# Kernel optimization log

Hardware: AMD Instinct MI355X
Metric: run time of the kernel (lower is better)

## Reference

```python
import jax, jax.numpy as jnp
import numpy as np

NUM_SPARSE = 26
VOCAB = 100000
EMB = 64
B = 2048
DENSE = 13
NUM_FEA = NUM_SPARSE + 1  # 26 embeddings + bottom-MLP output


def _xavier(key, shape):
    fan_in, fan_out = shape[0], shape[1]
    lim = jnp.sqrt(6.0 / (fan_in + fan_out))
    return jax.random.uniform(key, shape, jnp.float32, -lim, lim)


def setup_inputs() -> dict:
    key = jax.random.key(0)
    ks = jax.random.split(key, 20)
    inp = {
        "dense": jax.random.normal(ks[0], (B, DENSE), jnp.float32),
        "cat_idx": jax.random.randint(ks[1], (B, NUM_SPARSE), 0, VOCAB, jnp.int32),
        # stacked EmbeddingBag tables (all same vocab -> one [26, V, 64] tensor)
        "tables": _xavier(ks[2], (VOCAB, EMB))[None] * jnp.ones((NUM_SPARSE, 1, 1), jnp.float32) * 0
                  + jax.random.normal(ks[3], (NUM_SPARSE, VOCAB, EMB), jnp.float32) * 0.01,
        # bottom MLP: 13 -> 512 -> 256 -> 64
        "bw0": _xavier(ks[4], (DENSE, 512)), "bb0": jnp.zeros((512,), jnp.float32),
        "bw1": _xavier(ks[5], (512, 256)),   "bb1": jnp.zeros((256,), jnp.float32),
        "bw2": _xavier(ks[6], (256, EMB)),   "bb2": jnp.zeros((EMB,), jnp.float32),
        # top MLP: 415 -> 1024 -> 512 -> 256 -> 1
        "tw0": _xavier(ks[7], (EMB + NUM_FEA * (NUM_FEA - 1) // 2, 1024)), "tb0": jnp.zeros((1024,), jnp.float32),
        "tw1": _xavier(ks[8], (1024, 512)),  "tb1": jnp.zeros((512,), jnp.float32),
        "tw2": _xavier(ks[9], (512, 256)),   "tb2": jnp.zeros((256,), jnp.float32),
        "tw3": _xavier(ks[10], (256, 1)),    "tb3": jnp.zeros((1,), jnp.float32),
    }
    return inp


def reference(dense, cat_idx, tables, bw0, bb0, bw1, bb1, bw2, bb2,
              tw0, tb0, tw1, tb1, tw2, tb2, tw3, tb3):
    # bottom MLP on dense features -> [B, EMB]
    h = jax.nn.relu(dense @ bw0 + bb0)
    h = jax.nn.relu(h @ bw1 + bb1)
    bot = jax.nn.relu(h @ bw2 + bb2)

    # EmbeddingBag (single index per bag, sum mode == plain gather): [B, 26, EMB]
    feat_ids = jnp.arange(NUM_SPARSE)[None, :]  # [1, 26]
    emb = tables[feat_ids, cat_idx]             # [B, 26, EMB]

    # dot interaction: batched Gram matrix then lower-triangular gather
    T = jnp.concatenate([bot[:, None, :], emb], axis=1)  # [B, 27, EMB]
    Z = jnp.einsum("bif,bjf->bij", T, T)                  # [B, 27, 27]
    li, lj = np.tril_indices(NUM_FEA, k=-1)               # 351 pairs
    Zflat = Z[:, li, lj]                                  # [B, 351]

    R = jnp.concatenate([bot, Zflat], axis=1)             # [B, 415]

    # top MLP
    r = jax.nn.relu(R @ tw0 + tb0)
    r = jax.nn.relu(r @ tw1 + tb1)
    r = jax.nn.relu(r @ tw2 + tb2)
    out = jax.nn.sigmoid(r @ tw3 + tb3)                   # [B, 1]
    return out
```

## Files before the change

### kernel.cpp

```cpp
#include <hip/hip_runtime.h>
#include <hip/hip_bf16.h>


#define BATCH 2048
#define VOCAB 100000
#define EMB 64
#define NSPARSE 26
#define NFEA 27
#define NPAIR 351
#define RLD 448

typedef __attribute__((ext_vector_type(8))) __bf16 bf16x8;
typedef __attribute__((ext_vector_type(4))) float f32x4;
typedef __hip_bfloat16 bf16;

#define GLOAD16(g, l)                                                          \
    __builtin_amdgcn_global_load_lds(                                          \
        (const __attribute__((address_space(1))) unsigned int*)(g),            \
        (__attribute__((address_space(3))) unsigned int*)(l), 16, 0, 0)

template<int BK, bool DENSEPAD>
__global__ __launch_bounds__(256) void gemm_bf16(
    const void* __restrict__ Araw,
    const bf16* __restrict__ Wt,
    const float* __restrict__ bias,
    bf16* __restrict__ C,
    int M, int N, int K, int ldC)
{
    constexpr int ROWB   = BK * 2;
    constexpr int SLOTS  = BK / 8;
    constexpr int PASSES = BK / 32;
    constexpr int RPP    = 256 / SLOTS;

    __shared__ __align__(16) bf16 As[64 * BK];
    __shared__ __align__(16) bf16 Bs[64 * BK];

    const int t   = threadIdx.x;
    const int nbn = N >> 6;
    const int bm  = blockIdx.x / nbn;
    const int bn  = blockIdx.x % nbn;
    const int row0 = bm << 6, n0 = bn << 6;

    const int wid  = t >> 6, lane = t & 63;
    const int wr   = wid >> 1, wc = wid & 1;
    const int lr   = lane & 15;
    const int q    = lane >> 4;

#define SWZ(row, s) ((BK == 64) ? ((s) ^ ((row) & 7)) : ((s) ^ (((row) >> 1) & 3)))

    const int srow  = t / SLOTS;
    const int sslot = t % SLOTS;

    const bf16* Ab[PASSES];
    const bf16* Bb[PASSES];
#pragma unroll
    for (int p = 0; p < PASSES; ++p) {
        const int r = p * RPP + srow;
        const int g = SWZ(r, sslot);
        if (!DENSEPAD)
            Ab[p] = (const bf16*)Araw + (size_t)(row0 + r) * K + g * 8;
        Bb[p] = Wt + (size_t)(n0 + r) * K + g * 8;
    }

    f32x4 acc[2][2] = {};

    for (int k0 = 0; k0 < K; k0 += BK) {
        if (DENSEPAD) {
            const float* Df = (const float*)Araw;
#pragma unroll
            for (int idx = t; idx < 64 * 32; idx += 256) {
                const int r = idx >> 5, c = idx & 31;
                const float v = (c < 13) ? Df[(size_t)(row0 + r) * 13 + c] : 0.f;
                As[r * 32 + SWZ(r, c >> 3) * 8 + (c & 7)] = __float2bfloat16(v);
            }
        } else {
#pragma unroll
            for (int p = 0; p < PASSES; ++p)
                GLOAD16(Ab[p] + k0, (char*)As + p * 4096 + t * 16);
        }
#pragma unroll
        for (int p = 0; p < PASSES; ++p)
            GLOAD16(Bb[p] + k0, (char*)Bs + p * 4096 + t * 16);
        __syncthreads();

        bf16x8 af[PASSES][2], bfr[PASSES][2];
#pragma unroll
        for (int kk = 0; kk < PASSES; ++kk) {
#pragma unroll
            for (int m = 0; m < 2; ++m) {
                const int r = wr * 32 + 16 * m + lr;
                af[kk][m] = *(const bf16x8*)((const char*)As + r * ROWB +
                                             SWZ(r, kk * 4 + q) * 16);
            }
#pragma unroll
            for (int n = 0; n < 2; ++n) {
                const int r = wc * 32 + 16 * n + lr;
                bfr[kk][n] = *(const bf16x8*)((const char*)Bs + r * ROWB +
                                              SWZ(r, kk * 4 + q) * 16);
            }
        }
#pragma unroll
        for (int kk = 0; kk < PASSES; ++kk)
#pragma unroll
            for (int m = 0; m < 2; ++m)
#pragma unroll
                for (int n = 0; n < 2; ++n)
                    acc[m][n] = __builtin_amdgcn_mfma_f32_16x16x32_bf16(
                        af[kk][m], bfr[kk][n], acc[m][n], 0, 0, 0);
        __syncthreads();
    }
#undef SWZ

#pragma unroll
    for (int n = 0; n < 2; ++n) {
        const int col = n0 + wc * 32 + 16 * n + lr;
        const float bv = bias[col];
#pragma unroll
        for (int m = 0; m < 2; ++m) {
#pragma unroll
            for (int i = 0; i < 4; ++i) {
                const int row = row0 + wr * 32 + 16 * m + q * 4 + i;
                float v = acc[m][n][i] + bv;
                v = fmaxf(v, 0.f);
                C[(size_t)row * ldC + col] = __float2bfloat16(v);
            }
        }
    }
}

struct WConvArgs {
    const float* src[6];
    bf16*        dst[6];
    int K[6], N[6], Kp[6], t0[7];
};

__global__ __launch_bounds__(256) void wconv_kernel(WConvArgs a)
{
    __shared__ float Ts[32][33];
    int w = 0;
    while (w < 5 && (int)blockIdx.x >= a.t0[w + 1]) ++w;
    const int rel = blockIdx.x - a.t0[w];
    const int K = a.K[w], N = a.N[w], Kp = a.Kp[w];
    const int nbn = N >> 5;
    const int tk = rel / nbn, tn = rel % nbn;
    const int tx = threadIdx.x & 31, ty = threadIdx.x >> 5;

    const float* src = a.src[w];
    bf16* dst = a.dst[w];

#pragma unroll
    for (int rr = 0; rr < 4; ++rr) {
        const int k = tk * 32 + ty + rr * 8;
        const int n = tn * 32 + tx;
        Ts[ty + rr * 8][tx] = (k < K) ? src[(size_t)k * N + n] : 0.f;
    }
    __syncthreads();
#pragma unroll
    for (int rr = 0; rr < 4; ++rr) {
        const int n = tn * 32 + ty + rr * 8;
        const int kp = tk * 32 + tx;
        dst[(size_t)n * Kp + kp] = __float2bfloat16(Ts[tx][ty + rr * 8]);
    }
}

__global__ __launch_bounds__(256) void interact_kernel(
    const int* __restrict__ cat_idx, const float* __restrict__ tables,
    bf16* __restrict__ R)
{
    __shared__ float T[NFEA][EMB + 1];

    const int b    = blockIdx.x;
    const int t    = threadIdx.x;
    const int g    = t >> 6;
    const int lane = t & 63;
    bf16* Rrow = R + (size_t)b * RLD;

    for (int f = g; f < NFEA; f += 4) {
        if (f == 0) {
            T[0][lane] = __bfloat162float(Rrow[lane]);
        } else {
            const int j   = f - 1;
            const int idx = cat_idx[b * NSPARSE + j];
            T[f][lane] = tables[((size_t)j * VOCAB + idx) * EMB + lane];
        }
    }
    __syncthreads();

    if (t < RLD - 415) Rrow[415 + t] = __float2bfloat16(0.f);

    for (int p = t; p < NPAIR; p += 256) {
        int i = (int)((1.0f + sqrtf(1.0f + 8.0f * (float)p)) * 0.5f);
        while (i * (i - 1) / 2 > p) --i;
        while ((i + 1) * i / 2 <= p) ++i;
        const int j = p - i * (i - 1) / 2;
        float s = 0.f;
#pragma unroll 16
        for (int k = 0; k < EMB; ++k) s += T[i][k] * T[j][k];
        Rrow[EMB + p] = __float2bfloat16(s);
    }
}

__global__ __launch_bounds__(256) void top3_kernel(
    const bf16* __restrict__ A, const float* __restrict__ w,
    const float* __restrict__ bias, float* __restrict__ out)
{
    const int gid  = blockIdx.x * 256 + threadIdx.x;
    const int row  = gid >> 6;
    const int lane = gid & 63;

    const bf16* arow = A + (size_t)row * 256;
    float s = 0.f;
#pragma unroll
    for (int k = lane; k < 256; k += 64)
        s += __bfloat162float(arow[k]) * w[k];
#pragma unroll
    for (int off = 32; off; off >>= 1) s += __shfl_down(s, off);
    if (lane == 0) out[row] = 1.f / (1.f + expf(-(s + bias[0])));
}

extern "C" void kernel_launch(void* const* d_in, const int* in_sizes, int n_in,
                              void* d_out, int out_size, void* d_ws, size_t ws_size,
                              hipStream_t stream)
{
    const float* dense   = (const float*)d_in[0];
    const int*   cat_idx = (const int*)  d_in[1];
    const float* tables  = (const float*)d_in[2];
    const float* bw0 = (const float*)d_in[3];
    const float* bb0 = (const float*)d_in[4];
    const float* bw1 = (const float*)d_in[5];
    const float* bb1 = (const float*)d_in[6];
    const float* bw2 = (const float*)d_in[7];
    const float* bb2 = (const float*)d_in[8];
    const float* tw0 = (const float*)d_in[9];
    const float* tb0 = (const float*)d_in[10];
    const float* tw1 = (const float*)d_in[11];
    const float* tb1 = (const float*)d_in[12];
    const float* tw2 = (const float*)d_in[13];
    const float* tb2 = (const float*)d_in[14];
    const float* tw3 = (const float*)d_in[15];
    const float* tb3 = (const float*)d_in[16];

    bf16* p = (bf16*)d_ws;
    bf16* h0   = p; p += (size_t)BATCH * 512;
    bf16* h1   = p; p += (size_t)BATCH * 256;
    bf16* R    = p; p += (size_t)BATCH * RLD;
    bf16* r0   = p; p += (size_t)BATCH * 1024;
    bf16* r1   = p; p += (size_t)BATCH * 512;
    bf16* r2   = p; p += (size_t)BATCH * 256;
    bf16* bw0t = p; p += 512 * 32;
    bf16* bw1t = p; p += 256 * 512;
    bf16* bw2t = p; p += 64 * 256;
    bf16* tw0t = p; p += 1024 * RLD;
    bf16* tw1t = p; p += 512 * 1024;
    bf16* tw2t = p; p += 256 * 512;
    float* out = (float*)d_out;

    WConvArgs wa;
    wa.src[0] = bw0;  wa.dst[0] = bw0t; wa.K[0] = 13;   wa.N[0] = 512;  wa.Kp[0] = 32;
    wa.src[1] = bw1;  wa.dst[1] = bw1t; wa.K[1] = 512;  wa.N[1] = 256;  wa.Kp[1] = 512;
    wa.src[2] = bw2;  wa.dst[2] = bw2t; wa.K[2] = 256;  wa.N[2] = 64;   wa.Kp[2] = 256;
    wa.src[3] = tw0;  wa.dst[3] = tw0t; wa.K[3] = 415;  wa.N[3] = 1024; wa.Kp[3] = RLD;
    wa.src[4] = tw1;  wa.dst[4] = tw1t; wa.K[4] = 1024; wa.N[4] = 512;  wa.Kp[4] = 1024;
    wa.src[5] = tw2;  wa.dst[5] = tw2t; wa.K[5] = 512;  wa.N[5] = 256;  wa.Kp[5] = 512;
    int tiles = 0;
    for (int w = 0; w < 6; ++w) {
        wa.t0[w] = tiles;
        tiles += (wa.Kp[w] >> 5) * (wa.N[w] >> 5);
    }
    wa.t0[6] = tiles;

    wconv_kernel<<<tiles, 256, 0, stream>>>(wa);

    gemm_bf16<32, true ><<<(BATCH / 64) * (512 / 64), 256, 0, stream>>>(
        dense, bw0t, bb0, h0, BATCH, 512, 32, 512);
    gemm_bf16<64, false><<<(BATCH / 64) * (256 / 64), 256, 0, stream>>>(
        h0, bw1t, bb1, h1, BATCH, 256, 512, 256);
    gemm_bf16<64, false><<<(BATCH / 64) * (64 / 64), 256, 0, stream>>>(
        h1, bw2t, bb2, R, BATCH, 64, 256, RLD);

    interact_kernel<<<BATCH, 256, 0, stream>>>(cat_idx, tables, R);

    gemm_bf16<64, false><<<(BATCH / 64) * (1024 / 64), 256, 0, stream>>>(
        R, tw0t, tb0, r0, BATCH, 1024, RLD, 1024);
    gemm_bf16<64, false><<<(BATCH / 64) * (512 / 64), 256, 0, stream>>>(
        r0, tw1t, tb1, r1, BATCH, 512, 1024, 512);
    gemm_bf16<64, false><<<(BATCH / 64) * (256 / 64), 256, 0, stream>>>(
        r1, tw2t, tb2, r2, BATCH, 256, 512, 256);
    top3_kernel<<<BATCH / 4, 256, 0, stream>>>(r2, tw3, tb3, out);
}
```

Baseline: 67.74 us.

## Double-buffer GEMM LDS tiles and fuse bottom-MLP last layer into interaction

The GEMM kernel now double-buffers its A/B shared-memory tiles, prefetching the next K slice while computing on the current one, with one barrier per iteration. The final bottom-MLP layer (256->64) is removed as a separate GEMM launch and computed inside the interaction kernel with scalar FMAs from bf16 h1 and transposed weights. The interaction kernel also processes 8 batch rows per block with vectorized float4 embedding gathers. This saves a kernel launch and a round trip of the bottom output, but adds scalar dot-product work and far more shared memory per block (about 56KB for T), which may reduce occupancy.

```diff
diff --git a/kernel.cpp b/kernel.cpp
--- a/kernel.cpp
+++ b/kernel.cpp
@@ -19,6 +19,11 @@
         (const __attribute__((address_space(1))) unsigned int*)(g),            \
         (__attribute__((address_space(3))) unsigned int*)(l), 16, 0, 0)
 
+template<int BK>
+__device__ __forceinline__ int swz(int row, int s) {
+    return (BK == 64) ? (s ^ (row & 7)) : (s ^ ((row >> 1) & 3));
+}
+
 template<int BK, bool DENSEPAD>
 __global__ __launch_bounds__(256) void gemm_bf16(
     const void* __restrict__ Araw,
@@ -32,8 +37,8 @@
     constexpr int PASSES = BK / 32;
     constexpr int RPP    = 256 / SLOTS;
 
-    __shared__ __align__(16) bf16 As[64 * BK];
-    __shared__ __align__(16) bf16 Bs[64 * BK];
+    __shared__ __align__(16) bf16 As[2][64 * BK];
+    __shared__ __align__(16) bf16 Bs[2][64 * BK];
 
     const int t   = threadIdx.x;
     const int nbn = N >> 6;
@@ -46,8 +51,6 @@
     const int lr   = lane & 15;
     const int q    = lane >> 4;
 
-#define SWZ(row, s) ((BK == 64) ? ((s) ^ ((row) & 7)) : ((s) ^ (((row) >> 1) & 3)))
-
     const int srow  = t / SLOTS;
     const int sslot = t % SLOTS;
 
@@ -56,32 +59,40 @@
 #pragma unroll
     for (int p = 0; p < PASSES; ++p) {
         const int r = p * RPP + srow;
-        const int g = SWZ(r, sslot);
+        const int g = swz<BK>(r, sslot);
         if (!DENSEPAD)
             Ab[p] = (const bf16*)Araw + (size_t)(row0 + r) * K + g * 8;
         Bb[p] = Wt + (size_t)(n0 + r) * K + g * 8;
     }
 
-    f32x4 acc[2][2] = {};
-
-    for (int k0 = 0; k0 < K; k0 += BK) {
-        if (DENSEPAD) {
+    auto stage = [&](int k0, int buf) {
+        if constexpr (DENSEPAD) {
             const float* Df = (const float*)Araw;
 #pragma unroll
             for (int idx = t; idx < 64 * 32; idx += 256) {
                 const int r = idx >> 5, c = idx & 31;
                 const float v = (c < 13) ? Df[(size_t)(row0 + r) * 13 + c] : 0.f;
-                As[r * 32 + SWZ(r, c >> 3) * 8 + (c & 7)] = __float2bfloat16(v);
+                As[buf][r * 32 + swz<BK>(r, c >> 3) * 8 + (c & 7)] =
+                    __float2bfloat16(v);
             }
         } else {
 #pragma unroll
             for (int p = 0; p < PASSES; ++p)
-                GLOAD16(Ab[p] + k0, (char*)As + p * 4096 + t * 16);
+                GLOAD16(Ab[p] + k0, (char*)As[buf] + p * 4096 + t * 16);
         }
 #pragma unroll
         for (int p = 0; p < PASSES; ++p)
-            GLOAD16(Bb[p] + k0, (char*)Bs + p * 4096 + t * 16);
-        __syncthreads();
+            GLOAD16(Bb[p] + k0, (char*)Bs[buf] + p * 4096 + t * 16);
+    };
+
+    f32x4 acc[2][2] = {};
+
+    stage(0, 0);
+    __syncthreads();
+
+    int cur = 0;
+    for (int k0 = 0; k0 < K; k0 += BK) {
+        if (k0 + BK < K) stage(k0 + BK, cur ^ 1);
 
         bf16x8 af[PASSES][2], bfr[PASSES][2];
 #pragma unroll
@@ -89,14 +100,14 @@
 #pragma unroll
             for (int m = 0; m < 2; ++m) {
                 const int r = wr * 32 + 16 * m + lr;
-                af[kk][m] = *(const bf16x8*)((const char*)As + r * ROWB +
-                                             SWZ(r, kk * 4 + q) * 16);
+                af[kk][m] = *(const bf16x8*)((const char*)As[cur] + r * ROWB +
+                                             swz<BK>(r, kk * 4 + q) * 16);
             }
 #pragma unroll
             for (int n = 0; n < 2; ++n) {
                 const int r = wc * 32 + 16 * n + lr;
-                bfr[kk][n] = *(const bf16x8*)((const char*)Bs + r * ROWB +
-                                              SWZ(r, kk * 4 + q) * 16);
+                bfr[kk][n] = *(const bf16x8*)((const char*)Bs[cur] + r * ROWB +
+                                              swz<BK>(r, kk * 4 + q) * 16);
             }
         }
 #pragma unroll
@@ -107,9 +118,10 @@
                 for (int n = 0; n < 2; ++n)
                     acc[m][n] = __builtin_amdgcn_mfma_f32_16x16x32_bf16(
                         af[kk][m], bfr[kk][n], acc[m][n], 0, 0, 0);
+
         __syncthreads();
-    }
-#undef SWZ
+        cur ^= 1;
+    }
 
 #pragma unroll
     for (int n = 0; n < 2; ++n) {
@@ -164,39 +176,68 @@
 }
 
 __global__ __launch_bounds__(256) void interact_kernel(
-    const int* __restrict__ cat_idx, const float* __restrict__ tables,
+    const bf16* __restrict__ h1,
+    const bf16* __restrict__ bw2t,
+    const float* __restrict__ bb2,
+    const int* __restrict__ cat_idx,
+    const float* __restrict__ tables,
     bf16* __restrict__ R)
 {
-    __shared__ float T[NFEA][EMB + 1];
-
-    const int b    = blockIdx.x;
-    const int t    = threadIdx.x;
-    const int g    = t >> 6;
-    const int lane = t & 63;
-    bf16* Rrow = R + (size_t)b * RLD;
-
-    for (int f = g; f < NFEA; f += 4) {
-        if (f == 0) {
-            T[0][lane] = __bfloat162float(Rrow[lane]);
-        } else {
-            const int j   = f - 1;
-            const int idx = cat_idx[b * NSPARSE + j];
-            T[f][lane] = tables[((size_t)j * VOCAB + idx) * EMB + lane];
+    __shared__ float T[8][NFEA][EMB + 1];
+    __shared__ bf16  h1s[8][256];
+
+    const int b0 = blockIdx.x * 8;
+    const int t  = threadIdx.x;
+
+    {
+        const int r = t >> 5, c = (t & 31) * 8;
+        *(bf16x8*)&h1s[r][c] =
+            *(const bf16x8*)&h1[(size_t)(b0 + r) * 256 + c];
+    }
+
+    for (int l = t; l < 8 * NSPARSE * 16; l += 256) {
+        const int pair = l >> 4, c = (l & 15) * 4;
+        const int r = pair / NSPARSE, j = pair % NSPARSE;
+        const int idx = cat_idx[(b0 + r) * NSPARSE + j];
+        const float4 v =
+            *(const float4*)&tables[((size_t)j * VOCAB + idx) * EMB + c];
+        float* dst = &T[r][j + 1][c];
+        dst[0] = v.x; dst[1] = v.y; dst[2] = v.z; dst[3] = v.w;
+    }
+    __syncthreads();
+
+    for (int o = t; o < 512; o += 256) {
+        const int r = o >> 6, n = o & 63;
+        float s = bb2[n];
+        const bf16* wrow = bw2t + (size_t)n * 256;
+        for (int k = 0; k < 256; k += 8) {
+            const bf16x8 hv = *(const bf16x8*)&h1s[r][k];
+            const bf16x8 wv = *(const bf16x8*)&wrow[k];
+#pragma unroll
+            for (int u = 0; u < 8; ++u)
+                s += (float)hv[u] * (float)wv[u];
         }
+        s = fmaxf(s, 0.f);
+        T[r][0][n] = s;
+        R[(size_t)(b0 + r) * RLD + n] = __float2bfloat16(s);
+    }
+
+    for (int z = t; z < 8 * (RLD - 415); z += 256) {
+        const int r = z / (RLD - 415), c = z % (RLD - 415);
+        R[(size_t)(b0 + r) * RLD + 415 + c] = __float2bfloat16(0.f);
     }
     __syncthreads();
 
-    if (t < RLD - 415) Rrow[415 + t] = __float2bfloat16(0.f);
-
-    for (int p = t; p < NPAIR; p += 256) {
+    for (int task = t; task < 8 * NPAIR; task += 256) {
+        const int r = task / NPAIR, p = task % NPAIR;
         int i = (int)((1.0f + sqrtf(1.0f + 8.0f * (float)p)) * 0.5f);
         while (i * (i - 1) / 2 > p) --i;
         while ((i + 1) * i / 2 <= p) ++i;
         const int j = p - i * (i - 1) / 2;
         float s = 0.f;
 #pragma unroll 16
-        for (int k = 0; k < EMB; ++k) s += T[i][k] * T[j][k];
-        Rrow[EMB + p] = __float2bfloat16(s);
+        for (int k = 0; k < EMB; ++k) s += T[r][i][k] * T[r][j][k];
+        R[(size_t)(b0 + r) * RLD + EMB + p] = __float2bfloat16(s);
     }
 }
 
@@ -275,10 +316,9 @@
         dense, bw0t, bb0, h0, BATCH, 512, 32, 512);
     gemm_bf16<64, false><<<(BATCH / 64) * (256 / 64), 256, 0, stream>>>(
         h0, bw1t, bb1, h1, BATCH, 256, 512, 256);
-    gemm_bf16<64, false><<<(BATCH / 64) * (64 / 64), 256, 0, stream>>>(
-        h1, bw2t, bb2, R, BATCH, 64, 256, RLD);
-
-    interact_kernel<<<BATCH, 256, 0, stream>>>(cat_idx, tables, R);
+
+    interact_kernel<<<BATCH / 8, 256, 0, stream>>>(
+        h1, bw2t, bb2, cat_idx, tables, R);
 
     gemm_bf16<64, false><<<(BATCH / 64) * (1024 / 64), 256, 0, stream>>>(
         R, tw0t, tb0, r0, BATCH, 1024, RLD, 1024);
```

Result: slower. 76.87 us (+13.5%).
